# Kernel tuning notes

Hardware: AMD Instinct MI355X
Metric: run time of the kernel (lower is better)

Reference implementation:

```python
import jax, jax.numpy as jnp
import numpy as np

B = 32; N = 512; SEQ_LEN = 8
L = 0.05; T_REF = 5.0; V_TH = 20.0; V_RES = 0.0
SQL = float(np.sqrt(L))
BN_EPS = 1e-5

# ---- Dawson-style lookup tables for the LIF moment activation (built once, float64) ----
_XG = np.linspace(-10.0, 4.0, 7001)
_DX = _XG[1] - _XG[0]

def _cumtrapz(y):
    return np.concatenate([[0.0], np.cumsum(0.5 * (y[1:] + y[:-1]) * _DX)])

_phi = np.exp(-_XG ** 2)
_I = np.exp(-100.0) / 20.0 + _cumtrapz(_phi)          # int_{-inf}^x e^{-t^2} dt (asymptotic tail at -10)
_g = np.exp(_XG ** 2) * _I                             # 1st Dawson-like function g(x)
_G = _cumtrapz(_g)                                     # int g dx (rel. to -10)
_h = np.exp(_XG ** 2) * _cumtrapz(_phi * _g ** 2)      # 2nd Dawson-like function h(x)
_H = _cumtrapz(_h)                                     # int h dx

XG = jnp.asarray(_XG, jnp.float32)
GT = jnp.asarray(_g, jnp.float32)
GI = jnp.asarray(_G, jnp.float32)
HI = jnp.asarray(_H, jnp.float32)

def _interp(x, tab):
    return jnp.interp(x, XG, tab)

def moment_activate(u, s, rho):
    # Mnn_Activate_Mean / Std / Corr: LIF moment activation
    s = jnp.maximum(s, 1e-6)
    ub = jnp.clip((V_TH * L - u) / (s * SQL), -10.0, 4.0)
    lb = jnp.clip((V_RES * L - u) / (s * SQL), -10.0, 4.0)
    dG = _interp(ub, GI) - _interp(lb, GI)
    ua = 1.0 / (T_REF + (2.0 / L) * dG)                               # mean firing rate
    dH = jnp.maximum(_interp(ub, HI) - _interp(lb, HI), 0.0)
    sa = jnp.sqrt((8.0 / L ** 2) * dH * ua ** 3)                      # firing std
    dg = _interp(ub, GT) - _interp(lb, GT)
    chi = ua ** 2 * (2.0 / L) * dg / (SQL * jnp.maximum(sa, 1e-9))    # linear response coeff
    eye = jnp.eye(rho.shape[-1], dtype=rho.dtype)
    rho_out = chi[:, :, None] * chi[:, None, :] * rho                 # [B,N,N]
    rho_out = rho_out * (1.0 - eye) + eye                             # unit diagonal
    return ua, sa, rho_out

def linear_corr(W, b, u, s, rho):
    # Mnn_Linear_Corr: mean via affine map, covariance via W C W^T
    u_out = u @ W.T + b
    Cin = rho * s[:, :, None] * s[:, None, :]                         # [B,N,N] covariance
    C = jnp.einsum('bik,lk->bil', jnp.einsum('ij,bjk->bik', W, Cin), W)
    var = jnp.clip(jnp.diagonal(C, axis1=1, axis2=2), 0.0, None)
    s_out = jnp.sqrt(var)
    denom = s_out[:, :, None] * s_out[:, None, :]
    rho_out = jnp.where(denom > 1e-12, C / jnp.maximum(denom, 1e-12), 0.0)
    return u_out, s_out, rho_out

def mexi_hat(n, k=0.3):
    dx = 2.0 * np.pi / n
    x = np.arange(0.0, 2.0 * np.pi, dx)[:n]
    y = np.exp(2.0 * (np.cos(x) - 1.0)) * np.cos(2.0 * x)
    j = np.arange(n)
    idx = (j[None, :] - j[:, None]) % n                               # w[i,:] = y.roll(i)
    return y[idx].astype(np.float32)

def setup_inputs() -> dict:
    ks = jax.random.split(jax.random.key(0), 10)
    u = jax.random.normal(ks[0], (B, N), jnp.float32)
    s = jax.random.uniform(ks[1], (B, N), jnp.float32, 0.1, 1.0)
    A = jax.random.normal(ks[2], (B, N, N), jnp.float32) / np.sqrt(N)
    sym = 0.5 * (A + jnp.swapaxes(A, 1, 2))
    eye = jnp.eye(N, dtype=jnp.float32)
    rho = jnp.clip(sym, -0.5, 0.5) * (1.0 - eye) + eye                # valid-ish corr matrix
    u_ext = jax.random.normal(ks[3], (B, N), jnp.float32)
    s_ext = jax.random.uniform(ks[4], (B, N), jnp.float32, 0.1, 1.0)
    W = 0.02 * jax.random.normal(ks[5], (N, N), jnp.float32) + 0.1 * jnp.asarray(mexi_hat(N))
    b = 0.02 * jax.random.normal(ks[6], (N,), jnp.float32)
    W_ext = 0.02 * jax.random.normal(ks[7], (N, N), jnp.float32)
    b_ext = 0.02 * jax.random.normal(ks[8], (N,), jnp.float32)
    w_mean = 2.5 * jnp.ones((N,), jnp.float32)
    b_mean = 2.5 * jnp.ones((N,), jnp.float32)
    w_mean_ext = 2.5 * jnp.ones((N,), jnp.float32)
    b_mean_ext = 2.5 * jnp.ones((N,), jnp.float32)
    return {'u': u, 's': s, 'rho': rho, 'u_ext': u_ext, 's_ext': s_ext,
            'W': W, 'b': b, 'W_ext': W_ext, 'b_ext': b_ext,
            'w_mean': w_mean, 'b_mean': b_mean,
            'w_mean_ext': w_mean_ext, 'b_mean_ext': b_mean_ext,
            'seq_len': SEQ_LEN}

def reference(u, s, rho, u_ext, s_ext, W, b, W_ext, b_ext,
              w_mean, b_mean, w_mean_ext, b_mean_ext, seq_len):
    # external pathway (Mnn_Linear_without_Corr + BN), computed once
    u_e = u_ext @ W_ext.T + b_ext
    s_e = jnp.sqrt((s_ext ** 2) @ (W_ext ** 2).T)
    mean_e = jnp.mean(u_e, axis=0); var_e = jnp.var(u_e, axis=0)
    f_e = w_mean_ext / jnp.sqrt(var_e + BN_EPS)
    s_e = s_e * jnp.abs(f_e)                                          # Mnn_Std_Bn1d (uses pre-BN stats)
    u_e = (u_e - mean_e) * f_e + b_mean_ext

    def step(carry, _):
        u, s, rho = carry
        u, s, rho = linear_corr(W, b, u, s, rho)
        mean = jnp.mean(u, axis=0); var = jnp.var(u, axis=0)
        f = w_mean / jnp.sqrt(var + BN_EPS)
        s = s * jnp.abs(f)
        u = (u - mean) * f + b_mean
        u = u + u_e
        s = jnp.sqrt(s * s + s_e * s_e)
        return moment_activate(u, s, rho), None

    (u, s, rho), _ = jax.lax.scan(step, (u, s, rho), None, length=seq_len)
    return u, s, rho
```

## Files before the change

### kernel.cpp

```cpp
#include <hip/hip_runtime.h>
#include <math.h>


#define BB 32
#define NN 512
#define SEQ 8
#define TG 7001

typedef float f32x4 __attribute__((ext_vector_type(4)));
typedef short s16x8 __attribute__((ext_vector_type(8)));

#define GL16(g, l) __builtin_amdgcn_global_load_lds( \
    (const __attribute__((address_space(1))) void*)(g), \
    (__attribute__((address_space(3))) void*)(l), 16, 0, 0)

__device__ __forceinline__ unsigned short bf16_rne(float v) {
    unsigned u = __float_as_uint(v);
    u += 0x7FFFu + ((u >> 16) & 1u);
    return (unsigned short)(u >> 16);
}
__device__ __forceinline__ float bf16_f(unsigned short h) {
    return __uint_as_float(((unsigned)h) << 16);
}
__device__ __forceinline__ void split2(float v, unsigned short& h, unsigned short& l) {
    unsigned short hh = bf16_rne(v);
    h = hh;
    l = bf16_rne(v - bf16_f(hh));
}

__device__ __forceinline__ float interp_tab(const float* __restrict__ tab, float x) {
    float t = (x + 10.0f) * 500.0f;
    t = fminf(fmaxf(t, 0.0f), 7000.0f);
    int i0 = (int)t;
    if (i0 > 6999) i0 = 6999;
    float fr = t - (float)i0;
    float a = tab[i0];
    float b = tab[i0 + 1];
    return a + fr * (b - a);
}

__global__ void k_exp(double* __restrict__ expP, double* __restrict__ expM) {
    int k = blockIdx.x * 256 + threadIdx.x;
    if (k >= TG) return;
    double x = -10.0 + (14.0 / 7000.0) * k;
    expP[k] = exp(x * x);
    expM[k] = exp(-x * x);
}

__device__ double blk_exscan(double part, double* wsum) {
    int t = threadIdx.x, lane = t & 63, wid = t >> 6;
    double run = part;
    #pragma unroll
    for (int off = 1; off < 64; off <<= 1) {
        double nv = __shfl_up(run, off);
        if (lane >= off) run += nv;
    }
    if (lane == 63) wsum[wid] = run;
    __syncthreads();
    if (t < 16) {
        double v = wsum[t];
        #pragma unroll
        for (int off = 1; off < 16; off <<= 1) {
            double nv = __shfl_up(v, off);
            if (lane >= off) v += nv;
        }
        wsum[t] = v;
    }
    __syncthreads();
    double base = (wid > 0) ? wsum[wid - 1] : 0.0;
    double ex = base + run - part;
    __syncthreads();
    return ex;
}

__global__ __launch_bounds__(1024)
void k_scan(const double* __restrict__ expP, const double* __restrict__ expM,
            float* __restrict__ GT, float* __restrict__ GI, float* __restrict__ HI) {
    __shared__ double ys[7008];
    __shared__ double wsum[16];
    const int t = threadIdx.x;
    const double dx = 14.0 / 7000.0;
    int k0 = t * 7, k1 = k0 + 7;
    if (k1 > TG) k1 = TG;
    if (k0 > TG) k0 = TG;
    int kls = (k0 < 1) ? 1 : k0;

    for (int k = k0; k < k1; ++k) ys[k] = expM[k];
    __syncthreads();

    double tmp[7];
    {
        double part = 0.0;
        for (int k = kls; k < k1; ++k) part += 0.5 * (ys[k - 1] + ys[k]) * dx;
        double run = blk_exscan(part, wsum) + exp(-100.0) / 20.0;
        int c = 0;
        for (int k = k0; k < k1; ++k) {
            if (k >= 1) run += 0.5 * (ys[k - 1] + ys[k]) * dx;
            tmp[c] = expP[k] * run;
            GT[k] = (float)tmp[c];
            ++c;
        }
        __syncthreads();
        c = 0;
        for (int k = k0; k < k1; ++k) ys[k] = tmp[c++];
        __syncthreads();
    }
    {
        double part = 0.0;
        for (int k = kls; k < k1; ++k) part += 0.5 * (ys[k - 1] + ys[k]) * dx;
        double run = blk_exscan(part, wsum);
        for (int k = k0; k < k1; ++k) {
            if (k >= 1) run += 0.5 * (ys[k - 1] + ys[k]) * dx;
            GI[k] = (float)run;
        }
        __syncthreads();
    }
    {
        double part = 0.0;
        for (int k = kls; k < k1; ++k) {
            double ya = expM[k - 1] * ys[k - 1] * ys[k - 1];
            double yb = expM[k] * ys[k] * ys[k];
            part += 0.5 * (ya + yb) * dx;
        }
        double run = blk_exscan(part, wsum);
        int c = 0;
        for (int k = k0; k < k1; ++k) {
            if (k >= 1) {
                double ya = expM[k - 1] * ys[k - 1] * ys[k - 1];
                double yb = expM[k] * ys[k] * ys[k];
                run += 0.5 * (ya + yb) * dx;
            }
            tmp[c++] = run;
        }
        __syncthreads();
        c = 0;
        for (int k = k0; k < k1; ++k) ys[k] = tmp[c++];
        __syncthreads();
    }
    {
        double part = 0.0;
        for (int k = kls; k < k1; ++k)
            part += 0.5 * (expP[k - 1] * ys[k - 1] + expP[k] * ys[k]) * dx;
        double run = blk_exscan(part, wsum);
        for (int k = k0; k < k1; ++k) {
            if (k >= 1) run += 0.5 * (expP[k - 1] * ys[k - 1] + expP[k] * ys[k]) * dx;
            HI[k] = (float)run;
        }
    }
}

__global__ void k_splitW(const float* __restrict__ W,
                         unsigned short* __restrict__ Wh, unsigned short* __restrict__ Wl) {
    int idx = blockIdx.x * 256 + threadIdx.x;
    unsigned short h, l;
    split2(W[idx], h, l);
    Wh[idx] = h; Wl[idx] = l;
}

__global__ void k_splitQ(const float* __restrict__ rho, const float* __restrict__ s,
                         unsigned short* __restrict__ Qh, unsigned short* __restrict__ Ql) {
    size_t idx = (size_t)blockIdx.x * 256 + threadIdx.x;
    int b = (int)(idx >> 18);
    int i = (int)((idx >> 9) & 511);
    int j = (int)(idx & 511);
    float v = rho[idx] * s[b * NN + i] * s[b * NN + j];
    unsigned short h, l;
    split2(v, h, l);
    Qh[idx] = h; Ql[idx] = l;
}

template <int PHASE>
__global__ __launch_bounds__(256)
void gemm_step(const unsigned short* __restrict__ Ah, const unsigned short* __restrict__ Al,
               long aStride,
               const unsigned short* __restrict__ Bh, const unsigned short* __restrict__ Bl,
               long bStride,
               unsigned short* __restrict__ Oh, unsigned short* __restrict__ Ol,
               float* __restrict__ Of,
               const float* __restrict__ Wf, float* __restrict__ sv_a, float* __restrict__ sv_b,
               const float* __restrict__ u_prev, const float* __restrict__ bvec,
               float* __restrict__ u_lin,
               const float* __restrict__ bn_w, const float* __restrict__ bmv,
               const float* __restrict__ u_e, const float* __restrict__ s_e2,
               const float* __restrict__ GT, const float* __restrict__ GI,
               const float* __restrict__ HI,
               float* __restrict__ u_next, float* __restrict__ s_next) {
    __shared__ __align__(16) unsigned short As0[8192], As1[8192], Bs0[8192], Bs1[8192];
    __shared__ float slS[256], chS[256], snS[256];

    const int id = blockIdx.x;
    const int member = (id >> 3) & 3;
    const int g = (id & 7) | ((id >> 5) << 3);
    const int p = g & 3;
    const int b = g >> 2;
    const int xt = (PHASE == 0) ? p : member;
    const int yt = (PHASE == 0) ? member : p;
    const int i0 = yt * 128, j0 = xt * 128;
    const int tid = threadIdx.x;
    const int w = tid >> 6, lane = tid & 63;
    const int wqm = w >> 1, wqn = w & 1;
    const int kg = lane >> 4;

    const unsigned short* Abh = Ah + (size_t)b * aStride;
    const unsigned short* Abl = Al + (size_t)b * aStride;
    const unsigned short* Bbh = Bh + (size_t)b * bStride;
    const unsigned short* Bbl = Bl + (size_t)b * bStride;

    const size_t lgoff = ((size_t)(lane >> 2) * NN) + (size_t)((((lane & 3) ^ ((lane >> 3) & 3)) << 3));
    const int cxor = ((kg ^ (((lane & 15) >> 1) & 3)) << 3);

    auto stage = [&](int pp, int k0) {
        const int bufo = pp * 4096;
        #pragma unroll
        for (int inst = 0; inst < 2; ++inst) {
            const int br = w * 32 + inst * 16;
            GL16(Abh + (size_t)(i0 + br) * NN + k0 + lgoff, As0 + bufo + br * 32);
            GL16(Abl + (size_t)(i0 + br) * NN + k0 + lgoff, As1 + bufo + br * 32);
            GL16(Bbh + (size_t)(j0 + br) * NN + k0 + lgoff, Bs0 + bufo + br * 32);
            GL16(Bbl + (size_t)(j0 + br) * NN + k0 + lgoff, Bs1 + bufo + br * 32);
        }
    };
    stage(0, 0);

    if (PHASE == 0) {
        const int tile16 = yt * 4 + xt;
        const int row = tile16 * 32 + (tid >> 3);
        const int seg = tid & 7;
        const float4* wr = (const float4*)(Wf + (size_t)row * NN + seg * 64);
        const float4* ur = (const float4*)(u_prev + b * NN + seg * 64);
        float a0 = 0.f, a1 = 0.f, a2 = 0.f, a3 = 0.f;
        #pragma unroll
        for (int kk = 0; kk < 16; ++kk) {
            float4 wv = wr[kk], uv = ur[kk];
            a0 = fmaf(wv.x, uv.x, a0);
            a1 = fmaf(wv.y, uv.y, a1);
            a2 = fmaf(wv.z, uv.z, a2);
            a3 = fmaf(wv.w, uv.w, a3);
        }
        float au = (a0 + a1) + (a2 + a3);
        au += __shfl_xor(au, 1);
        au += __shfl_xor(au, 2);
        au += __shfl_xor(au, 4);
        if (seg == 0) u_lin[b * NN + row] = au + bvec[row];
    } else {
        const int ii = (tid < 128) ? (i0 + tid) : (j0 + tid - 128);
        float m = 0.0f;
        for (int bb = 0; bb < BB; ++bb) m += u_lin[bb * NN + ii];
        m *= (1.0f / BB);
        float v = 0.0f;
        for (int bb = 0; bb < BB; ++bb) {
            float d = u_lin[bb * NN + ii] - m;
            v = fmaf(d, d, v);
        }
        v *= (1.0f / BB);
        float f = bn_w[ii] / sqrtf(v + 1e-5f);
        const int idx = b * NN + ii;
        float s_l = sqrtf(fmaxf(sv_a[idx], 0.0f));
        float un = (u_lin[idx] - m) * f + bmv[ii] + u_e[idx];
        float sn = sqrtf(s_l * s_l * f * f + s_e2[idx]);
        const float SQL = 0.22360679774997896f;
        float ss = fmaxf(sn, 1e-6f);
        float inv = 1.0f / (ss * SQL);
        float ubx = fminf(fmaxf((1.0f - un) * inv, -10.0f), 4.0f);
        float lbx = fminf(fmaxf((0.0f - un) * inv, -10.0f), 4.0f);
        float dG = interp_tab(GI, ubx) - interp_tab(GI, lbx);
        float ua = 1.0f / (5.0f + 40.0f * dG);
        float dH = fmaxf(interp_tab(HI, ubx) - interp_tab(HI, lbx), 0.0f);
        float sa = sqrtf(3200.0f * dH * ua * ua * ua);
        float dg2 = interp_tab(GT, ubx) - interp_tab(GT, lbx);
        float ch = ua * ua * 40.0f * dg2 / (SQL * fmaxf(sa, 1e-9f));
        slS[tid] = s_l;
        chS[tid] = ch;
        snS[tid] = sa;
        if (i0 == j0 && tid < 128) {
            u_next[idx] = ua;
            s_next[idx] = sa;
            sv_b[idx] = 0.0f;
        }
    }
    __syncthreads();

    f32x4 acc[4][4];
    #pragma unroll
    for (int m2 = 0; m2 < 4; ++m2)
        #pragma unroll
        for (int n2 = 0; n2 < 4; ++n2) acc[m2][n2] = (f32x4){0.f, 0.f, 0.f, 0.f};

    for (int it = 0; it < 16; ++it) {
        if (it < 15) stage((it + 1) & 1, (it + 1) * 32);
        const int bufo = (it & 1) * 4096;
        s16x8 ahf[4], alf[4], bhf[4], blf[4];
        #pragma unroll
        for (int t = 0; t < 4; ++t) {
            const int ao = bufo + (wqm * 64 + t * 16 + (lane & 15)) * 32 + cxor;
            ahf[t] = *reinterpret_cast<const s16x8*>(&As0[ao]);
            alf[t] = *reinterpret_cast<const s16x8*>(&As1[ao]);
            const int bo = bufo + (wqn * 64 + t * 16 + (lane & 15)) * 32 + cxor;
            bhf[t] = *reinterpret_cast<const s16x8*>(&Bs0[bo]);
            blf[t] = *reinterpret_cast<const s16x8*>(&Bs1[bo]);
        }
        #pragma unroll
        for (int m2 = 0; m2 < 4; ++m2)
            #pragma unroll
            for (int n2 = 0; n2 < 4; ++n2) {
                acc[m2][n2] = __builtin_amdgcn_mfma_f32_16x16x32_bf16(ahf[m2], bhf[n2], acc[m2][n2], 0, 0, 0);
                acc[m2][n2] = __builtin_amdgcn_mfma_f32_16x16x32_bf16(ahf[m2], blf[n2], acc[m2][n2], 0, 0, 0);
                acc[m2][n2] = __builtin_amdgcn_mfma_f32_16x16x32_bf16(alf[m2], bhf[n2], acc[m2][n2], 0, 0, 0);
            }
        __syncthreads();
    }

    const size_t bofs = (size_t)b * NN * NN;

    if (PHASE == 0) {
        const int rb0 = i0 + wqm * 64 + (lane >> 4) * 4;
        const int cb0 = j0 + wqn * 64 + (lane & 15);
        float dp[16];
        #pragma unroll
        for (int m2 = 0; m2 < 4; ++m2)
            #pragma unroll
            for (int r = 0; r < 4; ++r) {
                int row = rb0 + m2 * 16 + r;
                const float* wrow = Wf + ((size_t)row << 9) + cb0;
                float s = 0.0f;
                #pragma unroll
                for (int n2 = 0; n2 < 4; ++n2) s = fmaf(acc[m2][n2][r], wrow[n2 * 16], s);
                dp[m2 * 4 + r] = s;
            }
        #pragma unroll
        for (int k = 0; k < 16; ++k) {
            #pragma unroll
            for (int off = 1; off < 16; off <<= 1) dp[k] += __shfl_xor(dp[k], off);
        }
        if ((lane & 15) == 0) {
            #pragma unroll
            for (int k = 0; k < 16; ++k) {
                int row = rb0 + (k >> 2) * 16 + (k & 3);
                atomicAdd(&sv_a[b * NN + row], dp[k]);
            }
        }
        #pragma unroll
        for (int m2 = 0; m2 < 4; ++m2)
            #pragma unroll
            for (int n2 = 0; n2 < 4; ++n2) {
                int col = cb0 + n2 * 16;
                #pragma unroll
                for (int r = 0; r < 4; ++r) {
                    int row = rb0 + m2 * 16 + r;
                    size_t idx = bofs + ((size_t)row << 9) + col;
                    unsigned short h, l;
                    split2(acc[m2][n2][r], h, l);
                    Oh[idx] = h; Ol[idx] = l;
                }
            }
    } else {
        const int lrb = wqm * 64 + (lane >> 4) * 4;
        const int lcb = wqn * 64 + (lane & 15);
        #pragma unroll
        for (int m2 = 0; m2 < 4; ++m2)
            #pragma unroll
            for (int r = 0; r < 4; ++r) {
                const int lr = lrb + m2 * 16 + r;
                const float si = slS[lr], ci = chS[lr], qi = snS[lr];
                const int row = i0 + lr;
                #pragma unroll
                for (int n2 = 0; n2 < 4; ++n2) {
                    const int lc = lcb + n2 * 16;
                    const float sj = slS[128 + lc], cj = chS[128 + lc], qj = snS[128 + lc];
                    const int col = j0 + lc;
                    float denom = si * sj;
                    float rv = (denom > 1e-12f) ? (acc[m2][n2][r] / fmaxf(denom, 1e-12f)) : 0.0f;
                    rv *= ci * cj;
                    if (row == col) rv = 1.0f;
                    size_t idx = bofs + ((size_t)row << 9) + col;
                    if (PHASE == 1) {
                        unsigned short h, l;
                        split2(rv * qi * qj, h, l);
                        Oh[idx] = h; Ol[idx] = l;
                    } else {
                        Of[idx] = rv;
                    }
                }
            }
    }
}

__global__ void k_ext_dots(const float* __restrict__ Wx, const float* __restrict__ bx,
                           const float* __restrict__ ux, const float* __restrict__ sx,
                           float* __restrict__ u_e, float* __restrict__ s_e2) {
    int gw = (blockIdx.x << 2) + (threadIdx.x >> 6);
    int lane = threadIdx.x & 63;
    int b = gw >> 9, i = gw & 511;
    const float* wr = Wx + (size_t)i * NN;
    const float* ub = ux + b * NN;
    const float* sb = sx + b * NN;
    float au = 0.0f, as2 = 0.0f;
    for (int j = lane; j < NN; j += 64) {
        float w = wr[j];
        float s = sb[j];
        au = fmaf(w, ub[j], au);
        as2 = fmaf(w * w, s * s, as2);
    }
    #pragma unroll
    for (int off = 32; off; off >>= 1) {
        au += __shfl_down(au, off);
        as2 += __shfl_down(as2, off);
    }
    if (lane == 0) {
        u_e[b * NN + i] = au + bx[i];
        s_e2[b * NN + i] = as2;
    }
}

__global__ void k_ext_stats(float* __restrict__ u_e, float* __restrict__ s_e2,
                            const float* __restrict__ wmx, const float* __restrict__ bmx) {
    int i = blockIdx.x * blockDim.x + threadIdx.x;
    if (i >= NN) return;
    float m = 0.0f;
    for (int b = 0; b < BB; ++b) m += u_e[b * NN + i];
    m *= (1.0f / BB);
    float v = 0.0f;
    for (int b = 0; b < BB; ++b) {
        float d = u_e[b * NN + i] - m;
        v = fmaf(d, d, v);
    }
    v *= (1.0f / BB);
    float f = wmx[i] / sqrtf(v + 1e-5f);
    float bm = bmx[i];
    for (int b = 0; b < BB; ++b) {
        u_e[b * NN + i] = (u_e[b * NN + i] - m) * f + bm;
        s_e2[b * NN + i] *= f * f;
    }
}

extern "C" void kernel_launch(void* const* d_in, const int* in_sizes, int n_in,
                              void* d_out, int out_size, void* d_ws, size_t ws_size,
                              hipStream_t stream) {
    (void)in_sizes; (void)n_in; (void)out_size; (void)ws_size;
    const float* u_in       = (const float*)d_in[0];
    const float* s_in       = (const float*)d_in[1];
    const float* rho_in     = (const float*)d_in[2];
    const float* u_ext      = (const float*)d_in[3];
    const float* s_ext      = (const float*)d_in[4];
    const float* W          = (const float*)d_in[5];
    const float* bvec       = (const float*)d_in[6];
    const float* W_ext      = (const float*)d_in[7];
    const float* b_ext      = (const float*)d_in[8];
    const float* w_mean     = (const float*)d_in[9];
    const float* b_mean     = (const float*)d_in[10];
    const float* w_mean_ext = (const float*)d_in[11];
    const float* b_mean_ext = (const float*)d_in[12];

    float* out_u   = (float*)d_out;
    float* out_s   = out_u + BB * NN;
    float* out_rho = out_s + BB * NN;
    unsigned short* Qh = (unsigned short*)out_rho;
    unsigned short* Ql = Qh + (size_t)BB * NN * NN;

    char* base = (char*)d_ws;
    size_t off = 0;
    auto alloc = [&](size_t bytes) -> char* {
        char* ptr = base + off;
        off += (bytes + 255) & ~(size_t)255;
        return ptr;
    };
    unsigned short* T1h = (unsigned short*)alloc((size_t)BB * NN * NN * 2);
    unsigned short* T1l = (unsigned short*)alloc((size_t)BB * NN * NN * 2);
    unsigned short* Wh  = (unsigned short*)alloc((size_t)NN * NN * 2);
    unsigned short* Wl  = (unsigned short*)alloc((size_t)NN * NN * 2);
    double* expP = (double*)alloc(TG * 8);
    double* expM = (double*)alloc(TG * 8);
    float* GTt   = (float*)alloc(TG * 4);
    float* GIt   = (float*)alloc(TG * 4);
    float* HIt   = (float*)alloc(TG * 4);
    float* u_e   = (float*)alloc(BB * NN * 4);
    float* s_e2  = (float*)alloc(BB * NN * 4);
    float* uA    = (float*)alloc(BB * NN * 4);
    float* uB2   = (float*)alloc(BB * NN * 4);
    float* sA    = (float*)alloc(BB * NN * 4);
    float* sB2   = (float*)alloc(BB * NN * 4);
    float* u_lin = (float*)alloc(BB * NN * 4);
    float* sv0   = (float*)alloc(BB * NN * 4);
    float* sv1   = (float*)alloc(BB * NN * 4);

    k_exp<<<28, 256, 0, stream>>>(expP, expM);
    k_scan<<<1, 1024, 0, stream>>>(expP, expM, GTt, GIt, HIt);
    k_splitW<<<NN * NN / 256, 256, 0, stream>>>(W, Wh, Wl);
    k_splitQ<<<BB * NN * NN / 256, 256, 0, stream>>>(rho_in, s_in, Qh, Ql);
    k_ext_dots<<<BB * NN / 4, 256, 0, stream>>>(W_ext, b_ext, u_ext, s_ext, u_e, s_e2);
    k_ext_stats<<<2, 256, 0, stream>>>(u_e, s_e2, w_mean_ext, b_mean_ext);
    (void)hipMemsetAsync(sv0, 0, BB * NN * 4, stream);

    const float* cu = u_in;

    for (int t = 0; t < SEQ; ++t) {
        float* sva = (t & 1) ? sv1 : sv0;
        float* svb = (t & 1) ? sv0 : sv1;
        gemm_step<0><<<512, 256, 0, stream>>>(
            Wh, Wl, 0L, Qh, Ql, (long)NN * NN, T1h, T1l, nullptr,
            W, sva, nullptr, cu, bvec, u_lin,
            nullptr, nullptr, nullptr, nullptr, nullptr, nullptr, nullptr,
            nullptr, nullptr);
        float* nu = (t == SEQ - 1) ? out_u : ((t & 1) ? uA : uB2);
        float* ns = (t == SEQ - 1) ? out_s : ((t & 1) ? sA : sB2);
        if (t < SEQ - 1) {
            gemm_step<1><<<512, 256, 0, stream>>>(
                T1h, T1l, (long)NN * NN, Wh, Wl, 0L, Qh, Ql, nullptr,
                nullptr, sva, svb, nullptr, nullptr, u_lin,
                w_mean, b_mean, u_e, s_e2, GTt, GIt, HIt, nu, ns);
        } else {
            gemm_step<2><<<512, 256, 0, stream>>>(
                T1h, T1l, (long)NN * NN, Wh, Wl, 0L, nullptr, nullptr, out_rho,
                nullptr, sva, svb, nullptr, nullptr, u_lin,
                w_mean, b_mean, u_e, s_e2, GTt, GIt, HIt, nu, ns);
        }
        cu = nu;
    }
}
```

Measured before the change: 788.1 us.

## Store bf16 operands in MFMA-fragment tiled layout and load directly from global

Reorders the split hi/lo bf16 matrices (W, Q, and intermediate T1/Q outputs) into a tiled layout where each 16-row by 32-k block is laid out exactly as MFMA fragments, so each lane reads a contiguous 16-byte vector. The GEMM kernel drops the LDS double-buffered staging and its per-iteration barriers, loading fragments straight from global memory (relying on L2/cache reuse across blocks), and sets launch bounds to allow two blocks per CU. This removes LDS traffic and synchronisation but gives up explicit shared-memory reuse between waves and exposes global-load latency without software pipelining.

```diff
diff --git a/kernel.cpp b/kernel.cpp
--- a/kernel.cpp
+++ b/kernel.cpp
@@ -10,10 +10,6 @@
 typedef float f32x4 __attribute__((ext_vector_type(4)));
 typedef short s16x8 __attribute__((ext_vector_type(8)));
 
-#define GL16(g, l) __builtin_amdgcn_global_load_lds( \
-    (const __attribute__((address_space(1))) void*)(g), \
-    (__attribute__((address_space(3))) void*)(l), 16, 0, 0)
-
 __device__ __forceinline__ unsigned short bf16_rne(float v) {
     unsigned u = __float_as_uint(v);
     u += 0x7FFFu + ((u >> 16) & 1u);
@@ -26,6 +22,10 @@
     unsigned short hh = bf16_rne(v);
     h = hh;
     l = bf16_rne(v - bf16_f(hh));
+}
+
+__device__ __forceinline__ size_t ts_idx(int r, int k) {
+    return (size_t)(((r >> 4) * 16 + (k >> 5)) * 512 + ((k >> 3) & 3) * 128 + (r & 15) * 8 + (k & 7));
 }
 
 __device__ __forceinline__ float interp_tab(const float* __restrict__ tab, float x) {
@@ -151,41 +151,61 @@
 
 __global__ void k_splitW(const float* __restrict__ W,
                          unsigned short* __restrict__ Wh, unsigned short* __restrict__ Wl) {
-    int idx = blockIdx.x * 256 + threadIdx.x;
-    unsigned short h, l;
-    split2(W[idx], h, l);
-    Wh[idx] = h; Wl[idx] = l;
+    int t = blockIdx.x * 256 + threadIdx.x;
+    int r = t >> 6, c8 = t & 63;
+    int k = c8 * 8;
+    const float* src = W + (size_t)r * NN + k;
+    s16x8 hv, lv;
+    #pragma unroll
+    for (int q = 0; q < 8; ++q) {
+        unsigned short h, l;
+        split2(src[q], h, l);
+        hv[q] = (short)h; lv[q] = (short)l;
+    }
+    size_t o = ts_idx(r, k);
+    *reinterpret_cast<s16x8*>(Wh + o) = hv;
+    *reinterpret_cast<s16x8*>(Wl + o) = lv;
 }
 
 __global__ void k_splitQ(const float* __restrict__ rho, const float* __restrict__ s,
                          unsigned short* __restrict__ Qh, unsigned short* __restrict__ Ql) {
-    size_t idx = (size_t)blockIdx.x * 256 + threadIdx.x;
-    int b = (int)(idx >> 18);
-    int i = (int)((idx >> 9) & 511);
-    int j = (int)(idx & 511);
-    float v = rho[idx] * s[b * NN + i] * s[b * NN + j];
-    unsigned short h, l;
-    split2(v, h, l);
-    Qh[idx] = h; Ql[idx] = l;
+    int t = blockIdx.x * 256 + threadIdx.x;
+    int b = t >> 15;
+    int rem = t & 32767;
+    int r = rem >> 6, c8 = rem & 63;
+    int k = c8 * 8;
+    const float* src = rho + ((size_t)b * NN + r) * NN + k;
+    const float* sb = s + b * NN;
+    float si = sb[r];
+    s16x8 hv, lv;
+    #pragma unroll
+    for (int q = 0; q < 8; ++q) {
+        float v = src[q] * si * sb[k + q];
+        unsigned short h, l;
+        split2(v, h, l);
+        hv[q] = (short)h; lv[q] = (short)l;
+    }
+    size_t o = (size_t)b * NN * NN + ts_idx(r, k);
+    *reinterpret_cast<s16x8*>(Qh + o) = hv;
+    *reinterpret_cast<s16x8*>(Ql + o) = lv;
 }
 
 template <int PHASE>
-__global__ __launch_bounds__(256)
-void gemm_step(const unsigned short* __restrict__ Ah, const unsigned short* __restrict__ Al,
-               long aStride,
-               const unsigned short* __restrict__ Bh, const unsigned short* __restrict__ Bl,
-               long bStride,
-               unsigned short* __restrict__ Oh, unsigned short* __restrict__ Ol,
-               float* __restrict__ Of,
-               const float* __restrict__ Wf, float* __restrict__ sv_a, float* __restrict__ sv_b,
-               const float* __restrict__ u_prev, const float* __restrict__ bvec,
-               float* __restrict__ u_lin,
-               const float* __restrict__ bn_w, const float* __restrict__ bmv,
-               const float* __restrict__ u_e, const float* __restrict__ s_e2,
-               const float* __restrict__ GT, const float* __restrict__ GI,
-               const float* __restrict__ HI,
-               float* __restrict__ u_next, float* __restrict__ s_next) {
-    __shared__ __align__(16) unsigned short As0[8192], As1[8192], Bs0[8192], Bs1[8192];
+__global__ __launch_bounds__(256, 2)
+void gemm_ts(const unsigned short* __restrict__ Ah, const unsigned short* __restrict__ Al,
+             long aStride,
+             const unsigned short* __restrict__ Bh, const unsigned short* __restrict__ Bl,
+             long bStride,
+             unsigned short* __restrict__ Oh, unsigned short* __restrict__ Ol,
+             float* __restrict__ Of,
+             const float* __restrict__ Wf, float* __restrict__ sv_a, float* __restrict__ sv_b,
+             const float* __restrict__ u_prev, const float* __restrict__ bvec,
+             float* __restrict__ u_lin,
+             const float* __restrict__ bn_w, const float* __restrict__ bmv,
+             const float* __restrict__ u_e, const float* __restrict__ s_e2,
+             const float* __restrict__ GT, const float* __restrict__ GI,
+             const float* __restrict__ HI,
+             float* __restrict__ u_next, float* __restrict__ s_next) {
     __shared__ float slS[256], chS[256], snS[256];
 
     const int id = blockIdx.x;
@@ -199,28 +219,6 @@
     const int tid = threadIdx.x;
     const int w = tid >> 6, lane = tid & 63;
     const int wqm = w >> 1, wqn = w & 1;
-    const int kg = lane >> 4;
-
-    const unsigned short* Abh = Ah + (size_t)b * aStride;
-    const unsigned short* Abl = Al + (size_t)b * aStride;
-    const unsigned short* Bbh = Bh + (size_t)b * bStride;
-    const unsigned short* Bbl = Bl + (size_t)b * bStride;
-
-    const size_t lgoff = ((size_t)(lane >> 2) * NN) + (size_t)((((lane & 3) ^ ((lane >> 3) & 3)) << 3));
-    const int cxor = ((kg ^ (((lane & 15) >> 1) & 3)) << 3);
-
-    auto stage = [&](int pp, int k0) {
-        const int bufo = pp * 4096;
-        #pragma unroll
-        for (int inst = 0; inst < 2; ++inst) {
-            const int br = w * 32 + inst * 16;
-            GL16(Abh + (size_t)(i0 + br) * NN + k0 + lgoff, As0 + bufo + br * 32);
-            GL16(Abl + (size_t)(i0 + br) * NN + k0 + lgoff, As1 + bufo + br * 32);
-            GL16(Bbh + (size_t)(j0 + br) * NN + k0 + lgoff, Bs0 + bufo + br * 32);
-            GL16(Bbl + (size_t)(j0 + br) * NN + k0 + lgoff, Bs1 + bufo + br * 32);
-        }
-    };
-    stage(0, 0);
 
     if (PHASE == 0) {
         const int tile16 = yt * 4 + xt;
@@ -277,8 +275,14 @@
             s_next[idx] = sa;
             sv_b[idx] = 0.0f;
         }
-    }
-    __syncthreads();
+        __syncthreads();
+    }
+
+    const int laneo = lane * 8;
+    const unsigned short* pAh = Ah + (size_t)b * aStride + (size_t)((i0 >> 4) + wqm * 4) * 8192 + laneo;
+    const unsigned short* pAl = Al + (size_t)b * aStride + (size_t)((i0 >> 4) + wqm * 4) * 8192 + laneo;
+    const unsigned short* pBh = Bh + (size_t)b * bStride + (size_t)((j0 >> 4) + wqn * 4) * 8192 + laneo;
+    const unsigned short* pBl = Bl + (size_t)b * bStride + (size_t)((j0 >> 4) + wqn * 4) * 8192 + laneo;
 
     f32x4 acc[4][4];
     #pragma unroll
@@ -286,18 +290,16 @@
         #pragma unroll
         for (int n2 = 0; n2 < 4; ++n2) acc[m2][n2] = (f32x4){0.f, 0.f, 0.f, 0.f};
 
-    for (int it = 0; it < 16; ++it) {
-        if (it < 15) stage((it + 1) & 1, (it + 1) * 32);
-        const int bufo = (it & 1) * 4096;
+    #pragma unroll 2
+    for (int kb = 0; kb < 16; ++kb) {
+        const int off = kb * 512;
         s16x8 ahf[4], alf[4], bhf[4], blf[4];
         #pragma unroll
         for (int t = 0; t < 4; ++t) {
-            const int ao = bufo + (wqm * 64 + t * 16 + (lane & 15)) * 32 + cxor;
-            ahf[t] = *reinterpret_cast<const s16x8*>(&As0[ao]);
-            alf[t] = *reinterpret_cast<const s16x8*>(&As1[ao]);
-            const int bo = bufo + (wqn * 64 + t * 16 + (lane & 15)) * 32 + cxor;
-            bhf[t] = *reinterpret_cast<const s16x8*>(&Bs0[bo]);
-            blf[t] = *reinterpret_cast<const s16x8*>(&Bs1[bo]);
+            ahf[t] = *reinterpret_cast<const s16x8*>(pAh + t * 8192 + off);
+            alf[t] = *reinterpret_cast<const s16x8*>(pAl + t * 8192 + off);
+            bhf[t] = *reinterpret_cast<const s16x8*>(pBh + t * 8192 + off);
+            blf[t] = *reinterpret_cast<const s16x8*>(pBl + t * 8192 + off);
         }
         #pragma unroll
         for (int m2 = 0; m2 < 4; ++m2)
@@ -307,14 +309,13 @@
                 acc[m2][n2] = __builtin_amdgcn_mfma_f32_16x16x32_bf16(ahf[m2], blf[n2], acc[m2][n2], 0, 0, 0);
                 acc[m2][n2] = __builtin_amdgcn_mfma_f32_16x16x32_bf16(alf[m2], bhf[n2], acc[m2][n2], 0, 0, 0);
             }
-        __syncthreads();
     }
 
     const size_t bofs = (size_t)b * NN * NN;
+    const int rb0 = i0 + wqm * 64 + (lane >> 4) * 4;
+    const int cb0 = j0 + wqn * 64 + (lane & 15);
 
     if (PHASE == 0) {
-        const int rb0 = i0 + wqm * 64 + (lane >> 4) * 4;
-        const int cb0 = j0 + wqn * 64 + (lane & 15);
         float dp[16];
         #pragma unroll
         for (int m2 = 0; m2 < 4; ++m2)
@@ -347,7 +348,7 @@
                 #pragma unroll
                 for (int r = 0; r < 4; ++r) {
                     int row = rb0 + m2 * 16 + r;
-                    size_t idx = bofs + ((size_t)row << 9) + col;
+                    size_t idx = bofs + ts_idx(row, col);
                     unsigned short h, l;
                     split2(acc[m2][n2][r], h, l);
                     Oh[idx] = h; Ol[idx] = l;
@@ -372,13 +373,13 @@
                     float rv = (denom > 1e-12f) ? (acc[m2][n2][r] / fmaxf(denom, 1e-12f)) : 0.0f;
                     rv *= ci * cj;
                     if (row == col) rv = 1.0f;
-                    size_t idx = bofs + ((size_t)row << 9) + col;
                     if (PHASE == 1) {
+                        size_t idx = bofs + ts_idx(row, col);
                         unsigned short h, l;
                         split2(rv * qi * qj, h, l);
                         Oh[idx] = h; Ol[idx] = l;
                     } else {
-                        Of[idx] = rv;
+                        Of[bofs + ((size_t)row << 9) + col] = rv;
                     }
                 }
             }
@@ -485,8 +486,8 @@
 
     k_exp<<<28, 256, 0, stream>>>(expP, expM);
     k_scan<<<1, 1024, 0, stream>>>(expP, expM, GTt, GIt, HIt);
-    k_splitW<<<NN * NN / 256, 256, 0, stream>>>(W, Wh, Wl);
-    k_splitQ<<<BB * NN * NN / 256, 256, 0, stream>>>(rho_in, s_in, Qh, Ql);
+    k_splitW<<<128, 256, 0, stream>>>(W, Wh, Wl);
+    k_splitQ<<<4096, 256, 0, stream>>>(rho_in, s_in, Qh, Ql);
     k_ext_dots<<<BB * NN / 4, 256, 0, stream>>>(W_ext, b_ext, u_ext, s_ext, u_e, s_e2);
     k_ext_stats<<<2, 256, 0, stream>>>(u_e, s_e2, w_mean_ext, b_mean_ext);
     (void)hipMemsetAsync(sv0, 0, BB * NN * 4, stream);
@@ -496,7 +497,7 @@
     for (int t = 0; t < SEQ; ++t) {
         float* sva = (t & 1) ? sv1 : sv0;
         float* svb = (t & 1) ? sv0 : sv1;
-        gemm_step<0><<<512, 256, 0, stream>>>(
+        gemm_ts<0><<<512, 256, 0, stream>>>(
             Wh, Wl, 0L, Qh, Ql, (long)NN * NN, T1h, T1l, nullptr,
             W, sva, nullptr, cu, bvec, u_lin,
             nullptr, nullptr, nullptr, nullptr, nullptr, nullptr, nullptr,
@@ -504,12 +505,12 @@
         float* nu = (t == SEQ - 1) ? out_u : ((t & 1) ? uA : uB2);
         float* ns = (t == SEQ - 1) ? out_s : ((t & 1) ? sA : sB2);
         if (t < SEQ - 1) {
-            gemm_step<1><<<512, 256, 0, stream>>>(
+            gemm_ts<1><<<512, 256, 0, stream>>>(
                 T1h, T1l, (long)NN * NN, Wh, Wl, 0L, Qh, Ql, nullptr,
                 nullptr, sva, svb, nullptr, nullptr, u_lin,
                 w_mean, b_mean, u_e, s_e2, GTt, GIt, HIt, nu, ns);
         } else {
-            gemm_step<2><<<512, 256, 0, stream>>>(
+            gemm_ts<2><<<512, 256, 0, stream>>>(
                 T1h, T1l, (long)NN * NN, Wh, Wl, 0L, nullptr, nullptr, out_rho,
                 nullptr, sva, svb, nullptr, nullptr, u_lin,
                 w_mean, b_mean, u_e, s_e2, GTt, GIt, HIt, nu, ns);
```

New measurement: 959.8 us. +21.8%, slower.
